# Kernel optimization log

Measured on AMD Instinct MI355X. Metric: run time of the kernel, lower is better.

Reference implementation:

```python
import jax, jax.numpy as jnp
import numpy as np

PH = PW = 7          # pooled output size
SR = 2               # sampling_ratio: SR x SR samples per bin
SCALES = (0.25, 0.125, 0.0625, 0.03125)  # FPN strides 4,8,16,32
K = 512              # number of ROIs
B = 2                # batch (images)
IMG = 800.0


def _coords(start, bsize, P):
    # sample coords for P bins, SR samples per bin: start + p*bin + (i+0.5)*bin/SR
    j = jnp.arange(P * SR, dtype=start.dtype)
    return (start[:, None]
            + (j // SR)[None, :] * bsize[:, None]
            + ((j % SR) + 0.5)[None, :] * (bsize[:, None] / SR))  # [K, P*SR]


def _roi_align_level(feat, rois, scale):
    # feat: [B, C, H, W] ; rois: [K, 5] (batch_idx, x1, y1, x2, y2 in image coords)
    Bf, C, H, W = feat.shape
    b = rois[:, 0].astype(jnp.int32)
    x1 = rois[:, 1] * scale
    y1 = rois[:, 2] * scale
    x2 = rois[:, 3] * scale
    y2 = rois[:, 4] * scale
    roi_w = jnp.maximum(x2 - x1, 1.0)   # legacy (aligned=False) ROIAlign
    roi_h = jnp.maximum(y2 - y1, 1.0)
    ys = _coords(y1, roi_h / PH, PH)    # [K, Sy]
    xs = _coords(x1, roi_w / PW, PW)    # [K, Sx]
    y = ys[:, :, None]                  # [K, Sy, 1]
    x = xs[:, None, :]                  # [K, 1, Sx]
    valid = (y > -1.0) & (y < H) & (x > -1.0) & (x < W)  # [K, Sy, Sx]
    yc = jnp.clip(y, 0.0, None)
    xc = jnp.clip(x, 0.0, None)
    yl = jnp.minimum(yc.astype(jnp.int32), H - 1)
    xl = jnp.minimum(xc.astype(jnp.int32), W - 1)
    yh = jnp.minimum(yl + 1, H - 1)
    xh = jnp.minimum(xl + 1, W - 1)
    ly = jnp.where(yl >= H - 1, 0.0, yc - yl)
    lx = jnp.where(xl >= W - 1, 0.0, xc - xl)
    hy, hx = 1.0 - ly, 1.0 - lx
    feat_flat = feat.reshape(Bf, C, H * W)
    Sy, Sx = PH * SR, PW * SR
    acc = jnp.zeros((rois.shape[0], C, Sy, Sx), feat.dtype)
    corners = ((yl, xl, hy * hx), (yl, xh, hy * lx),
               (yh, xl, ly * hx), (yh, xh, ly * lx))
    for yy, xx, w in corners:  # fixed 4-corner loop (not a data-dim loop)
        idx = jnp.broadcast_to(yy * W + xx, (rois.shape[0], Sy, Sx))
        vals = jax.vmap(lambda bi, ii: jnp.take(feat_flat, bi, axis=0)[:, ii])(b, idx)
        acc = acc + vals * jnp.broadcast_to(w, idx.shape)[:, None, :, :]
    acc = jnp.where(valid[:, None, :, :], acc, 0.0)
    # average SRxSR samples within each 7x7 bin
    return acc.reshape(rois.shape[0], C, PH, SR, PW, SR).mean(axis=(3, 5))


def setup_inputs() -> dict:
    key = jax.random.key(0)
    ks = jax.random.split(key, 10)
    input_0 = jax.random.normal(ks[0], (B, 256, 200, 200), jnp.float32)
    input_1 = jax.random.normal(ks[1], (B, 256, 100, 100), jnp.float32)
    input_2 = jax.random.normal(ks[2], (B, 256, 50, 50), jnp.float32)
    input_3 = jax.random.normal(ks[3], (B, 256, 25, 25), jnp.float32)
    bidx = jax.random.randint(ks[4], (K,), 0, B).astype(jnp.float32)
    x1 = jax.random.uniform(ks[5], (K,)) * (IMG - 64.0)
    y1 = jax.random.uniform(ks[6], (K,)) * (IMG - 64.0)
    bw = 32.0 + jax.random.uniform(ks[7], (K,)) * 200.0
    bh = 32.0 + jax.random.uniform(ks[8], (K,)) * 200.0
    rois = jnp.stack([bidx, x1, y1,
                      jnp.minimum(x1 + bw, IMG),
                      jnp.minimum(y1 + bh, IMG)], axis=1).astype(jnp.float32)
    level = jax.random.randint(ks[9], (K,), 0, 4).astype(jnp.int32)
    rois_counts = jnp.array([K // 2, K - K // 2], jnp.int32)  # unused (all ROIs valid)
    return {"input_0": input_0, "input_1": input_1, "input_2": input_2,
            "input_3": input_3, "rois": rois, "rois_counts": rois_counts,
            "level": level}


def reference(input_0, input_1, input_2, input_3, rois, rois_counts, level):
    feats = (input_0, input_1, input_2, input_3)
    lvl = level.astype(jnp.int32)
    out = jnp.zeros((rois.shape[0], input_0.shape[1], PH, PW), input_0.dtype)
    for i, (f, s) in enumerate(zip(feats, SCALES)):
        o = _roi_align_level(f, rois, s)
        out = out + jnp.where((lvl == i)[:, None, None, None], o, 0.0)
    return out
```

## Files before the change

kernel.cpp:

```cpp
#include <hip/hip_runtime.h>


#define NUM_CH 256
#define CPT    4
#define CGRP   64

typedef float floatx2 __attribute__((ext_vector_type(2)));
typedef float floatx4 __attribute__((ext_vector_type(4)));

__device__ __forceinline__ float ext4(floatx4 v, int i) {
    float r = (i == 1) ? v.y : v.x;
    r = (i == 2) ? v.z : r;
    r = (i == 3) ? v.w : r;
    return r;
}

__global__ __launch_bounds__(256) void roi_align_kernel(
    const float* __restrict__ f0,
    const float* __restrict__ f1,
    const float* __restrict__ f2,
    const float* __restrict__ f3,
    const float* __restrict__ rois_f,
    const int* __restrict__ level,
    float* __restrict__ out,
    int K,
    int NW)
{
    int nb  = gridDim.x;
    int q   = nb >> 3, r = nb & 7;
    int xcd = blockIdx.x & 7;
    int idx = blockIdx.x >> 3;
    int l   = xcd * q + min(xcd, r) + idx;

    int wid = l * 4 + (int)(threadIdx.x >> 6);
    if (wid >= NW) return;
    int lane = threadIdx.x & 63;
    if (lane >= 49) return;

    int k  = wid % K;
    int c2 = wid / K;
    k  = __builtin_amdgcn_readfirstlane(k);
    c2 = __builtin_amdgcn_readfirstlane(c2);

    int p  = lane;
    int ph = p / 7;
    int pw = p % 7;

    int lvl = level[k];
    const float* f;
    int H, W; float scale;
    if (lvl == 0)      { f = f0; H = 200; W = 200; scale = 0.25f;    }
    else if (lvl == 1) { f = f1; H = 100; W = 100; scale = 0.125f;   }
    else if (lvl == 2) { f = f2; H = 50;  W = 50;  scale = 0.0625f;  }
    else               { f = f3; H = 25;  W = 25;  scale = 0.03125f; }

    const float* rf = rois_f + (size_t)k * 5;
    float r0 = rf[0];
    float x1 = rf[1] * scale, y1 = rf[2] * scale;
    float x2 = rf[3] * scale, y2 = rf[4] * scale;
    int bi = (int)r0;
    bi = (bi < 0) ? 0 : ((bi > 1) ? 1 : bi);

    float bh = fmaxf(y2 - y1, 1.0f) * (1.0f / 7.0f);
    float bw = fmaxf(x2 - x1, 1.0f) * (1.0f / 7.0f);

    const size_t plane = (size_t)(H * W);
    const float* base  = f + ((size_t)bi * NUM_CH + c2) * plane;
    const size_t cstr  = (size_t)CGRP * plane;

    int   rA[2], rB[2];
    float lyv[2], hyv[2], vy[2];
    #pragma unroll
    for (int sy = 0; sy < 2; ++sy) {
        float y = y1 + (float)ph * bh + ((float)sy + 0.5f) * (bh * 0.5f);
        bool valid = (y > -1.0f) && (y < (float)H);
        float yc = fmaxf(y, 0.0f);
        int yl = min((int)yc, H - 1);
        int yh = min(yl + 1, H - 1);
        float ly = (yl >= H - 1) ? 0.0f : (yc - (float)yl);
        rA[sy] = yl * W;
        rB[sy] = yh * W;
        lyv[sy] = ly; hyv[sy] = 1.0f - ly;
        vy[sy] = valid ? 0.25f : 0.0f;
    }
    int   xlv[2], xhv[2];
    float lxv[2], hxv[2], vx[2];
    #pragma unroll
    for (int sx = 0; sx < 2; ++sx) {
        float x = x1 + (float)pw * bw + ((float)sx + 0.5f) * (bw * 0.5f);
        bool valid = (x > -1.0f) && (x < (float)W);
        float xc = fmaxf(x, 0.0f);
        int xl = min((int)xc, W - 1);
        float lx = (xl >= W - 1) ? 0.0f : (xc - (float)xl);
        xlv[sx] = xl;
        xhv[sx] = min(xl + 1, W - 1);
        lxv[sx] = lx; hxv[sx] = 1.0f - lx;
        vx[sx] = valid ? 1.0f : 0.0f;
    }

    float acc[CPT];
    #pragma unroll
    for (int j = 0; j < CPT; ++j) acc[j] = 0.0f;

    if (bw <= 3.98f) {
        int xq = min(xlv[0], W - 4);
        int i0l = min(max(xlv[0] - xq, 0), 3);
        int i0h = min(max(xhv[0] - xq, 0), 3);
        int i1l = min(max(xlv[1] - xq, 0), 3);
        int i1h = min(max(xhv[1] - xq, 0), 3);

        #pragma unroll
        for (int sy = 0; sy < 2; ++sy) {
            floatx4 LA[CPT], LB[CPT];
            #pragma unroll
            for (int j = 0; j < CPT; ++j) {
                const float* bj = base + (size_t)j * cstr;
                LA[j] = *(const floatx4*)(bj + rA[sy] + xq);
                LB[j] = *(const floatx4*)(bj + rB[sy] + xq);
            }
            #pragma unroll
            for (int sx = 0; sx < 2; ++sx) {
                int il = sx ? i1l : i0l;
                int ih = sx ? i1h : i0h;
                float vs  = vy[sy] * vx[sx];
                float w00 = hyv[sy] * hxv[sx] * vs;
                float w01 = hyv[sy] * lxv[sx] * vs;
                float w10 = lyv[sy] * hxv[sx] * vs;
                float w11 = lyv[sy] * lxv[sx] * vs;
                #pragma unroll
                for (int j = 0; j < CPT; ++j) {
                    acc[j] += w00 * ext4(LA[j], il) + w01 * ext4(LA[j], ih)
                            + w10 * ext4(LB[j], il) + w11 * ext4(LB[j], ih);
                }
            }
        }
    } else {
        int   xb[2];
        float sel[2];
        #pragma unroll
        for (int sx = 0; sx < 2; ++sx) {
            int xq = min(xlv[sx], W - 2);
            xb[sx]  = xq;
            sel[sx] = (xlv[sx] > xq) ? 1.0f : 0.0f;
        }
        #pragma unroll
        for (int sy = 0; sy < 2; ++sy) {
            floatx2 va[CPT][2], vb[CPT][2];
            #pragma unroll
            for (int sx = 0; sx < 2; ++sx) {
                #pragma unroll
                for (int j = 0; j < CPT; ++j) {
                    const float* bj = base + (size_t)j * cstr;
                    va[j][sx] = *(const floatx2*)(bj + rA[sy] + xb[sx]);
                    vb[j][sx] = *(const floatx2*)(bj + rB[sy] + xb[sx]);
                }
            }
            #pragma unroll
            for (int sx = 0; sx < 2; ++sx) {
                float vs  = vy[sy] * vx[sx];
                float w00 = hyv[sy] * hxv[sx] * vs;
                float w01 = hyv[sy] * lxv[sx] * vs;
                float w10 = lyv[sy] * hxv[sx] * vs;
                float w11 = lyv[sy] * lxv[sx] * vs;
                float s0  = sel[sx];
                #pragma unroll
                for (int j = 0; j < CPT; ++j) {
                    float v00 = va[j][sx].x + s0 * (va[j][sx].y - va[j][sx].x);
                    float v10 = vb[j][sx].x + s0 * (vb[j][sx].y - vb[j][sx].x);
                    acc[j] += w00 * v00 + w01 * va[j][sx].y
                            + w10 * v10 + w11 * vb[j][sx].y;
                }
            }
        }
    }

    size_t ob = ((size_t)k * NUM_CH + c2) * 49 + p;
    #pragma unroll
    for (int j = 0; j < CPT; ++j)
        out[ob + (size_t)j * (CGRP * 49)] = acc[j];
}

extern "C" void kernel_launch(void* const* d_in, const int* in_sizes, int n_in,
                              void* d_out, int out_size, void* d_ws, size_t ws_size,
                              hipStream_t stream) {
    const float* f0   = (const float*)d_in[0];
    const float* f1   = (const float*)d_in[1];
    const float* f2   = (const float*)d_in[2];
    const float* f3   = (const float*)d_in[3];
    const float* rois = (const float*)d_in[4];
    const int* level = (const int*)d_in[6];
    float* out = (float*)d_out;

    int K  = out_size / (NUM_CH * 49);
    int NW = K * CGRP;
    int threads = 256;
    int blocks  = (NW + 3) / 4;
    roi_align_kernel<<<blocks, threads, 0, stream>>>(f0, f1, f2, f3, rois, level, out, K, NW);
}
```

Before: 184.5 us.

## Pack all 64 lanes with (channel,bin) pairs and reuse rows when samples share a row

Work is redistributed so each wavefront covers 64 consecutive (channel, bin) pairs instead of 49 bins of a single channel. This removes the 15 idle lanes per wave and cuts the wave count from K*64 to K*49. It also reuses the loaded feature rows for the second y-sample when both samples fall on the same row, skipping redundant loads. In exchange, lanes within a wave now span two channels, so their feature gathers are less contiguous, and the bin index must be computed with a divide per lane.

```diff
diff --git a/kernel.cpp b/kernel.cpp
--- a/kernel.cpp
+++ b/kernel.cpp
@@ -4,6 +4,8 @@
 #define NUM_CH 256
 #define CPT    4
 #define CGRP   64
+#define WPR    49
+#define PAIRS  3136
 
 typedef float floatx2 __attribute__((ext_vector_type(2)));
 typedef float floatx4 __attribute__((ext_vector_type(4)));
@@ -35,14 +37,15 @@
     int wid = l * 4 + (int)(threadIdx.x >> 6);
     if (wid >= NW) return;
     int lane = threadIdx.x & 63;
-    if (lane >= 49) return;
-
-    int k  = wid % K;
-    int c2 = wid / K;
-    k  = __builtin_amdgcn_readfirstlane(k);
-    c2 = __builtin_amdgcn_readfirstlane(c2);
-
-    int p  = lane;
+
+    int k = wid % K;
+    int g = wid / K;
+    k = __builtin_amdgcn_readfirstlane(k);
+    g = __builtin_amdgcn_readfirstlane(g);
+
+    int pair = g * 64 + lane;
+    int c2   = pair / 49;
+    int p    = pair - c2 * 49;
     int ph = p / 7;
     int pw = p % 7;
 
@@ -98,6 +101,8 @@
         vx[sx] = valid ? 1.0f : 0.0f;
     }
 
+    bool same = (rA[1] == rA[0]);
+
     float acc[CPT];
     #pragma unroll
     for (int j = 0; j < CPT; ++j) acc[j] = 0.0f;
@@ -109,14 +114,22 @@
         int i1l = min(max(xlv[1] - xq, 0), 3);
         int i1h = min(max(xhv[1] - xq, 0), 3);
 
+        floatx4 LA[CPT], LB[CPT];
+        #pragma unroll
+        for (int j = 0; j < CPT; ++j) {
+            const float* bj = base + (size_t)j * cstr;
+            LA[j] = *(const floatx4*)(bj + rA[0] + xq);
+            LB[j] = *(const floatx4*)(bj + rB[0] + xq);
+        }
         #pragma unroll
         for (int sy = 0; sy < 2; ++sy) {
-            floatx4 LA[CPT], LB[CPT];
-            #pragma unroll
-            for (int j = 0; j < CPT; ++j) {
-                const float* bj = base + (size_t)j * cstr;
-                LA[j] = *(const floatx4*)(bj + rA[sy] + xq);
-                LB[j] = *(const floatx4*)(bj + rB[sy] + xq);
+            if (sy == 1 && !same) {
+                #pragma unroll
+                for (int j = 0; j < CPT; ++j) {
+                    const float* bj = base + (size_t)j * cstr;
+                    LA[j] = *(const floatx4*)(bj + rA[1] + xq);
+                    LB[j] = *(const floatx4*)(bj + rB[1] + xq);
+                }
             }
             #pragma unroll
             for (int sx = 0; sx < 2; ++sx) {
@@ -143,16 +156,27 @@
             xb[sx]  = xq;
             sel[sx] = (xlv[sx] > xq) ? 1.0f : 0.0f;
         }
+        floatx2 va[CPT][2], vb[CPT][2];
+        #pragma unroll
+        for (int sx = 0; sx < 2; ++sx) {
+            #pragma unroll
+            for (int j = 0; j < CPT; ++j) {
+                const float* bj = base + (size_t)j * cstr;
+                va[j][sx] = *(const floatx2*)(bj + rA[0] + xb[sx]);
+                vb[j][sx] = *(const floatx2*)(bj + rB[0] + xb[sx]);
+            }
+        }
         #pragma unroll
         for (int sy = 0; sy < 2; ++sy) {
-            floatx2 va[CPT][2], vb[CPT][2];
-            #pragma unroll
-            for (int sx = 0; sx < 2; ++sx) {
-                #pragma unroll
-                for (int j = 0; j < CPT; ++j) {
-                    const float* bj = base + (size_t)j * cstr;
-                    va[j][sx] = *(const floatx2*)(bj + rA[sy] + xb[sx]);
-                    vb[j][sx] = *(const floatx2*)(bj + rB[sy] + xb[sx]);
+            if (sy == 1 && !same) {
+                #pragma unroll
+                for (int sx = 0; sx < 2; ++sx) {
+                    #pragma unroll
+                    for (int j = 0; j < CPT; ++j) {
+                        const float* bj = base + (size_t)j * cstr;
+                        va[j][sx] = *(const floatx2*)(bj + rA[1] + xb[sx]);
+                        vb[j][sx] = *(const floatx2*)(bj + rB[1] + xb[sx]);
+                    }
                 }
             }
             #pragma unroll
@@ -174,10 +198,10 @@
         }
     }
 
-    size_t ob = ((size_t)k * NUM_CH + c2) * 49 + p;
+    size_t ob = (size_t)k * (NUM_CH * 49) + (size_t)g * 64 + lane;
     #pragma unroll
     for (int j = 0; j < CPT; ++j)
-        out[ob + (size_t)j * (CGRP * 49)] = acc[j];
+        out[ob + (size_t)j * PAIRS] = acc[j];
 }
 
 extern "C" void kernel_launch(void* const* d_in, const int* in_sizes, int n_in,
@@ -192,7 +216,7 @@
     float* out = (float*)d_out;
 
     int K  = out_size / (NUM_CH * 49);
-    int NW = K * CGRP;
+    int NW = K * WPR;
     int threads = 256;
     int blocks  = (NW + 3) / 4;
     roi_align_kernel<<<blocks, threads, 0, stream>>>(f0, f1, f2, f3, rois, level, out, K, NW);
```

After: 185.9 us. About the same (+0.7%).

## Transpose FPN levels 1-3 to channels-last workspace and gather with per-ROI blocks

Applied to the files above, without the earlier changes.

Feature maps for levels 1-3 are transposed into an HWC layout in the workspace, using LDS tiles inside the first kernel's extra blocks. Those blocks run alongside the level-0 gather, which keeps the old NCHW path. A second kernel handles ROIs on levels 1-3 with one block per ROI: each lane loads 4 contiguous channels per corner as a vector, and the 49x256 result is staged in LDS so stores to the output are coalesced. The aim is to replace scattered per-channel loads with contiguous channel vectors. The cost is an extra full pass over the level 1-3 feature maps and a second kernel launch.

```diff
diff --git a/kernel.cpp b/kernel.cpp
--- a/kernel.cpp
+++ b/kernel.cpp
@@ -2,8 +2,11 @@
 
 
 #define NUM_CH 256
-#define CPT    4
 #define CGRP   64
+#define OFF2   5120000
+#define OFF3   6400000
+#define WS_FLOATS 6720000
+#define TBLK_FULL 1400
 
 typedef float floatx2 __attribute__((ext_vector_type(2)));
 typedef float floatx4 __attribute__((ext_vector_type(4)));
@@ -15,7 +18,31 @@
     return r;
 }
 
-__global__ __launch_bounds__(256) void roi_align_kernel(
+template<int H, int W, int P>
+__device__ __forceinline__ void transpose_row(
+    const float* __restrict__ src, float* __restrict__ dst, int m, float* lds)
+{
+    int b  = m / (H * 4);
+    int rm = m - b * (H * 4);
+    int y  = rm >> 2;
+    int ct = rm & 3;
+    int tid = threadIdx.x;
+    const float* s = src + (((size_t)b * NUM_CH + ct * 64) * H + y) * W;
+    for (int i = tid; i < 64 * W; i += 256) {
+        int c = i / W;
+        int x = i - c * W;
+        lds[c * P + x] = s[(size_t)c * (H * W) + x];
+    }
+    __syncthreads();
+    float* d = dst + (((size_t)b * H + y) * (size_t)W) * NUM_CH + ct * 64;
+    for (int i = tid; i < W * 64; i += 256) {
+        int x = i >> 6;
+        int c = i & 63;
+        d[(size_t)x * NUM_CH + c] = lds[c * P + x];
+    }
+}
+
+__global__ __launch_bounds__(256) void k1_transpose_gather(
     const float* __restrict__ f0,
     const float* __restrict__ f1,
     const float* __restrict__ f2,
@@ -23,15 +50,26 @@
     const float* __restrict__ rois_f,
     const int* __restrict__ level,
     float* __restrict__ out,
-    int K,
-    int NW)
+    float* __restrict__ ws,
+    int K, int TBLK, int all_levels)
 {
-    int nb  = gridDim.x;
+    __shared__ float lds[64 * 101];
+    int bid = blockIdx.x;
+    if (bid < TBLK) {
+        if (bid < 800)       transpose_row<100, 100, 101>(f1, ws,        bid,        lds);
+        else if (bid < 1200) transpose_row<50,  50,  51 >(f2, ws + OFF2, bid - 800,  lds);
+        else                 transpose_row<25,  25,  27 >(f3, ws + OFF3, bid - 1200, lds);
+        return;
+    }
+
+    int nb  = gridDim.x - TBLK;
+    int lb  = bid - TBLK;
     int q   = nb >> 3, r = nb & 7;
-    int xcd = blockIdx.x & 7;
-    int idx = blockIdx.x >> 3;
+    int xcd = lb & 7;
+    int idx = lb >> 3;
     int l   = xcd * q + min(xcd, r) + idx;
 
+    int NW  = K * CGRP;
     int wid = l * 4 + (int)(threadIdx.x >> 6);
     if (wid >= NW) return;
     int lane = threadIdx.x & 63;
@@ -42,17 +80,19 @@
     k  = __builtin_amdgcn_readfirstlane(k);
     c2 = __builtin_amdgcn_readfirstlane(c2);
 
-    int p  = lane;
-    int ph = p / 7;
-    int pw = p % 7;
-
     int lvl = level[k];
+    if (!all_levels && lvl != 0) return;
+
     const float* f;
     int H, W; float scale;
     if (lvl == 0)      { f = f0; H = 200; W = 200; scale = 0.25f;    }
     else if (lvl == 1) { f = f1; H = 100; W = 100; scale = 0.125f;   }
     else if (lvl == 2) { f = f2; H = 50;  W = 50;  scale = 0.0625f;  }
     else               { f = f3; H = 25;  W = 25;  scale = 0.03125f; }
+
+    int p  = lane;
+    int ph = p / 7;
+    int pw = p % 7;
 
     const float* rf = rois_f + (size_t)k * 5;
     float r0 = rf[0];
@@ -98,9 +138,9 @@
         vx[sx] = valid ? 1.0f : 0.0f;
     }
 
-    float acc[CPT];
+    float acc[4];
     #pragma unroll
-    for (int j = 0; j < CPT; ++j) acc[j] = 0.0f;
+    for (int j = 0; j < 4; ++j) acc[j] = 0.0f;
 
     if (bw <= 3.98f) {
         int xq = min(xlv[0], W - 4);
@@ -111,9 +151,9 @@
 
         #pragma unroll
         for (int sy = 0; sy < 2; ++sy) {
-            floatx4 LA[CPT], LB[CPT];
-            #pragma unroll
-            for (int j = 0; j < CPT; ++j) {
+            floatx4 LA[4], LB[4];
+            #pragma unroll
+            for (int j = 0; j < 4; ++j) {
                 const float* bj = base + (size_t)j * cstr;
                 LA[j] = *(const floatx4*)(bj + rA[sy] + xq);
                 LB[j] = *(const floatx4*)(bj + rB[sy] + xq);
@@ -128,7 +168,7 @@
                 float w10 = lyv[sy] * hxv[sx] * vs;
                 float w11 = lyv[sy] * lxv[sx] * vs;
                 #pragma unroll
-                for (int j = 0; j < CPT; ++j) {
+                for (int j = 0; j < 4; ++j) {
                     acc[j] += w00 * ext4(LA[j], il) + w01 * ext4(LA[j], ih)
                             + w10 * ext4(LB[j], il) + w11 * ext4(LB[j], ih);
                 }
@@ -145,11 +185,11 @@
         }
         #pragma unroll
         for (int sy = 0; sy < 2; ++sy) {
-            floatx2 va[CPT][2], vb[CPT][2];
+            floatx2 va[4][2], vb[4][2];
             #pragma unroll
             for (int sx = 0; sx < 2; ++sx) {
                 #pragma unroll
-                for (int j = 0; j < CPT; ++j) {
+                for (int j = 0; j < 4; ++j) {
                     const float* bj = base + (size_t)j * cstr;
                     va[j][sx] = *(const floatx2*)(bj + rA[sy] + xb[sx]);
                     vb[j][sx] = *(const floatx2*)(bj + rB[sy] + xb[sx]);
@@ -164,7 +204,7 @@
                 float w11 = lyv[sy] * lxv[sx] * vs;
                 float s0  = sel[sx];
                 #pragma unroll
-                for (int j = 0; j < CPT; ++j) {
+                for (int j = 0; j < 4; ++j) {
                     float v00 = va[j][sx].x + s0 * (va[j][sx].y - va[j][sx].x);
                     float v10 = vb[j][sx].x + s0 * (vb[j][sx].y - vb[j][sx].x);
                     acc[j] += w00 * v00 + w01 * va[j][sx].y
@@ -176,8 +216,114 @@
 
     size_t ob = ((size_t)k * NUM_CH + c2) * 49 + p;
     #pragma unroll
-    for (int j = 0; j < CPT; ++j)
+    for (int j = 0; j < 4; ++j)
         out[ob + (size_t)j * (CGRP * 49)] = acc[j];
+}
+
+__global__ __launch_bounds__(256) void k2_gather_l123(
+    const float* __restrict__ rois_f,
+    const int* __restrict__ level,
+    const float* __restrict__ ws,
+    float* __restrict__ out,
+    int K)
+{
+    __shared__ float lds[49 * 257];
+    int k = blockIdx.x;
+    int lvl = level[k];
+    if (lvl == 0) return;
+
+    const float* t; int H, W; float scale;
+    if (lvl == 1)      { t = ws;        H = 100; W = 100; scale = 0.125f;   }
+    else if (lvl == 2) { t = ws + OFF2; H = 50;  W = 50;  scale = 0.0625f;  }
+    else               { t = ws + OFF3; H = 25;  W = 25;  scale = 0.03125f; }
+
+    const float* rf = rois_f + (size_t)k * 5;
+    float r0 = rf[0];
+    float x1 = rf[1] * scale, y1 = rf[2] * scale;
+    float x2 = rf[3] * scale, y2 = rf[4] * scale;
+    int bi = (int)r0;
+    bi = (bi < 0) ? 0 : ((bi > 1) ? 1 : bi);
+
+    float bh = fmaxf(y2 - y1, 1.0f) * (1.0f / 7.0f);
+    float bw = fmaxf(x2 - x1, 1.0f) * (1.0f / 7.0f);
+
+    const float* tb = t + (size_t)bi * H * W * NUM_CH;
+    int wave = threadIdx.x >> 6;
+    int lane = threadIdx.x & 63;
+    int cb   = lane * 4;
+
+    for (int px = wave; px < 49; px += 4) {
+        int ph = px / 7, pw = px % 7;
+
+        int rows[4]; float lyv[2], hyv[2], vy[2];
+        #pragma unroll
+        for (int sy = 0; sy < 2; ++sy) {
+            float y = y1 + (float)ph * bh + ((float)sy + 0.5f) * (bh * 0.5f);
+            bool valid = (y > -1.0f) && (y < (float)H);
+            float yc = fmaxf(y, 0.0f);
+            int yl = min((int)yc, H - 1);
+            int yh = min(yl + 1, H - 1);
+            float ly = (yl >= H - 1) ? 0.0f : (yc - (float)yl);
+            rows[2 * sy]     = yl;
+            rows[2 * sy + 1] = yh;
+            lyv[sy] = ly; hyv[sy] = 1.0f - ly;
+            vy[sy] = valid ? 0.25f : 0.0f;
+        }
+        int cols[4]; float lxv[2], hxv[2], vx[2];
+        #pragma unroll
+        for (int sx = 0; sx < 2; ++sx) {
+            float x = x1 + (float)pw * bw + ((float)sx + 0.5f) * (bw * 0.5f);
+            bool valid = (x > -1.0f) && (x < (float)W);
+            float xc = fmaxf(x, 0.0f);
+            int xl = min((int)xc, W - 1);
+            float lx = (xl >= W - 1) ? 0.0f : (xc - (float)xl);
+            cols[2 * sx]     = xl;
+            cols[2 * sx + 1] = min(xl + 1, W - 1);
+            lxv[sx] = lx; hxv[sx] = 1.0f - lx;
+            vx[sx] = valid ? 1.0f : 0.0f;
+        }
+
+        floatx4 v[4][4];
+        #pragma unroll
+        for (int rr = 0; rr < 4; ++rr) {
+            #pragma unroll
+            for (int cc = 0; cc < 4; ++cc) {
+                v[rr][cc] = *(const floatx4*)(
+                    tb + ((size_t)rows[rr] * W + cols[cc]) * NUM_CH + cb);
+            }
+        }
+
+        floatx4 acc = {0.0f, 0.0f, 0.0f, 0.0f};
+        #pragma unroll
+        for (int sy = 0; sy < 2; ++sy) {
+            #pragma unroll
+            for (int sx = 0; sx < 2; ++sx) {
+                float vs  = vy[sy] * vx[sx];
+                float w00 = hyv[sy] * hxv[sx] * vs;
+                float w01 = hyv[sy] * lxv[sx] * vs;
+                float w10 = lyv[sy] * hxv[sx] * vs;
+                float w11 = lyv[sy] * lxv[sx] * vs;
+                acc += v[2 * sy][2 * sx]     * w00;
+                acc += v[2 * sy][2 * sx + 1] * w01;
+                acc += v[2 * sy + 1][2 * sx]     * w10;
+                acc += v[2 * sy + 1][2 * sx + 1] * w11;
+            }
+        }
+
+        int lb = px * 257 + cb;
+        lds[lb + 0] = acc.x;
+        lds[lb + 1] = acc.y;
+        lds[lb + 2] = acc.z;
+        lds[lb + 3] = acc.w;
+    }
+    __syncthreads();
+
+    float* ob = out + (size_t)k * (NUM_CH * 49);
+    for (int i = threadIdx.x; i < NUM_CH * 49; i += 256) {
+        int c  = i / 49;
+        int px = i - c * 49;
+        ob[i] = lds[px * 257 + c];
+    }
 }
 
 extern "C" void kernel_launch(void* const* d_in, const int* in_sizes, int n_in,
@@ -191,9 +337,15 @@
     const int* level = (const int*)d_in[6];
     float* out = (float*)d_out;
 
-    int K  = out_size / (NUM_CH * 49);
-    int NW = K * CGRP;
-    int threads = 256;
-    int blocks  = (NW + 3) / 4;
-    roi_align_kernel<<<blocks, threads, 0, stream>>>(f0, f1, f2, f3, rois, level, out, K, NW);
-}
+    int K = out_size / (NUM_CH * 49);
+    int use_ws = (ws_size >= (size_t)WS_FLOATS * 4) ? 1 : 0;
+    int TBLK = use_ws ? TBLK_FULL : 0;
+    int GB   = K * 16;
+
+    k1_transpose_gather<<<TBLK + GB, 256, 0, stream>>>(
+        f0, f1, f2, f3, rois, level, out, (float*)d_ws, K, TBLK, use_ws ? 0 : 1);
+    if (use_ws) {
+        k2_gather_l123<<<K, 256, 0, stream>>>(
+            rois, level, (const float*)d_ws, out, K);
+    }
+}
```

After: 192.3 us. +4.2%, slower.
